# Optimization experiments

Hardware: AMD Instinct MI355X
Metric: run time of the kernel (lower is better)

## Reference

```python
import jax, jax.numpy as jnp
import numpy as np

B, MAXN, F, H, T, L = 32, 1024, 215, 256, 8, 3
N = B * MAXN            # 32768 global nodes
E = 524288              # total edges, global indices


def setup_inputs() -> dict:
    key = jax.random.key(0)
    ks = jax.random.split(key, 12)
    s = 0.05
    return {
        "node_features": jax.random.normal(ks[0], (B, MAXN, F), dtype=jnp.float32),
        "edge_index": jax.random.randint(ks[1], (2, E), 0, N, dtype=jnp.int32),
        "edge_type": jax.random.randint(ks[2], (E,), 0, T, dtype=jnp.int32),
        # input projection
        "Wp": jax.random.normal(ks[3], (H, F), dtype=jnp.float32) * s,
        "bp": jax.random.normal(ks[4], (H,), dtype=jnp.float32) * s,
        # per-layer, per-edge-type message linears
        "Wm": jax.random.normal(ks[5], (L, T, H, H), dtype=jnp.float32) * s,
        "bm": jax.random.normal(ks[6], (L, T, H), dtype=jnp.float32) * s,
        # per-layer GRUCell params (torch layout: [r|z|n] stacked, 3H rows)
        "Wih": jax.random.normal(ks[7], (L, 3 * H, H), dtype=jnp.float32) * s,
        "Whh": jax.random.normal(ks[8], (L, 3 * H, H), dtype=jnp.float32) * s,
        "bih": jax.random.normal(ks[9], (L, 3 * H), dtype=jnp.float32) * s,
        "bhh": jax.random.normal(ks[10], (L, 3 * H), dtype=jnp.float32) * s,
    }


def _gru_cell(x, h, Wih, Whh, bih, bhh):
    # torch.nn.GRUCell math
    gi = x @ Wih.T + bih            # (N, 3H)
    gh = h @ Whh.T + bhh            # (N, 3H)
    i_r, i_z, i_n = jnp.split(gi, 3, axis=-1)
    h_r, h_z, h_n = jnp.split(gh, 3, axis=-1)
    r = jax.nn.sigmoid(i_r + h_r)
    z = jax.nn.sigmoid(i_z + h_z)
    n = jnp.tanh(i_n + r * h_n)
    return (1.0 - z) * n + z * h


def reference(node_features, edge_index, edge_type, Wp, bp, Wm, bm, Wih, Whh, bih, bhh):
    # flatten batch of graphs into global node array, project to hidden
    h = node_features.reshape(-1, F) @ Wp.T + bp          # (N, H)
    src, dst = edge_index[0], edge_index[1]
    for l in range(L):
        # apply all T type-specific linears to every node once (equivalent to
        # the per-edge-type mask+gather+Linear loop), then gather per edge
        Ht = jnp.einsum('nd,ted->nte', h, Wm[l]) + bm[l]  # (N, T, H)
        msg = Ht[src, edge_type]                           # (E, H) gather
        m = jax.ops.segment_sum(msg, dst, num_segments=N)  # scatter-add (N, H)
        h = _gru_cell(m, h, Wih[l], Whh[l], bih[l], bhh[l])
        # dropout is identity in eval mode
    # readout: full graphs -> sum each graph's node block
    return h.reshape(B, MAXN, H).sum(axis=1)               # (B, H)
```

## Files before the change

### kernel.cpp

```cpp
#include <hip/hip_runtime.h>

#define N_NODES 32768
#define E_EDGES 524288
#define F_IN    215
#define H_DIM   256
#define T_TYPES 8
#define L_LAYERS 3
#define B_GRAPHS 32
#define MAXN_   1024
#define NT_BINS (N_NODES * T_TYPES)

typedef float  f32x4  __attribute__((ext_vector_type(4)));
typedef __bf16 bf16x8 __attribute__((ext_vector_type(8)));

__device__ __forceinline__ unsigned short f2bf(float f) {
  union { float f; unsigned u; } v; v.f = f;
  unsigned r = v.u + 0x7fffu + ((v.u >> 16) & 1u);
  return (unsigned short)(r >> 16);
}
__device__ __forceinline__ float bf2f(unsigned short h) {
  union { unsigned u; float f; } v; v.u = ((unsigned)h) << 16;
  return v.f;
}
__device__ __forceinline__ float bflo(unsigned u) { union { unsigned x; float f; } v; v.x = u << 16; return v.f; }
__device__ __forceinline__ float bfhi(unsigned u) { union { unsigned x; float f; } v; v.x = u & 0xffff0000u; return v.f; }

typedef const __attribute__((address_space(1))) unsigned int* gas_ptr;
typedef __attribute__((address_space(3))) unsigned int* las_ptr;
__device__ __forceinline__ void gload_lds16(const unsigned short* g, unsigned short* l) {
  __builtin_amdgcn_global_load_lds((gas_ptr)g, (las_ptr)l, 16, 0, 0);
}

__device__ __forceinline__ void acc16(float* a, const uint4 v, const uint4 w) {
  a[0]  += bflo(v.x); a[1]  += bfhi(v.x);
  a[2]  += bflo(v.y); a[3]  += bfhi(v.y);
  a[4]  += bflo(v.z); a[5]  += bfhi(v.z);
  a[6]  += bflo(v.w); a[7]  += bfhi(v.w);
  a[8]  += bflo(w.x); a[9]  += bfhi(w.x);
  a[10] += bflo(w.y); a[11] += bfhi(w.y);
  a[12] += bflo(w.z); a[13] += bfhi(w.z);
  a[14] += bflo(w.w); a[15] += bfhi(w.w);
}

static constexpr size_t OFF_BIG     = 0;
static constexpr size_t REL_CURSOR  = 1048576;
static constexpr size_t REL_BSUM    = 2097152;
static constexpr size_t REL_WPPAD   = 33554432;
static constexpr size_t REL_HALT    = 50331648;
static constexpr size_t REL_OFFS    = 100663296;
static constexpr size_t REL_SORTED  = 104857600;
static constexpr size_t OFF_H_B     = 134217728;
static constexpr size_t OFF_M_B     = 150994944;
static constexpr size_t OFF_WMB     = 167772160;
static constexpr size_t OFF_WIH     = 170917888;
static constexpr size_t OFF_WHH     = 172097536;
static constexpr size_t WS_REQUIRED = 173277184;

__global__ void hist_kernel(const int* __restrict__ dst, const int* __restrict__ et,
                            int* __restrict__ cnt) {
  int e = blockIdx.x * 256 + threadIdx.x;
  atomicAdd(&cnt[dst[e] * T_TYPES + et[e]], 1);
}

__global__ __launch_bounds__(1024) void scan1(const int* __restrict__ cnt,
                                              int* __restrict__ offs,
                                              int* __restrict__ bsum) {
  __shared__ int wsum[16];
  const int t = threadIdx.x, lane = t & 63, wid = t >> 6;
  const int idx = blockIdx.x * 1024 + t;
  const int v = cnt[idx];
  int x = v;
  #pragma unroll
  for (int off = 1; off < 64; off <<= 1) {
    int u = __shfl_up(x, off, 64);
    if (lane >= off) x += u;
  }
  if (lane == 63) wsum[wid] = x;
  __syncthreads();
  int wbase = 0;
  for (int i = 0; i < wid; ++i) wbase += wsum[i];
  offs[idx] = wbase + x - v;
  if (t == 1023) bsum[blockIdx.x] = wbase + x;
}

__global__ __launch_bounds__(256) void scan2(int* __restrict__ bsum) {
  __shared__ int wsum[4];
  const int t = threadIdx.x, lane = t & 63, wid = t >> 6;
  const int v = bsum[t];
  int x = v;
  #pragma unroll
  for (int off = 1; off < 64; off <<= 1) {
    int u = __shfl_up(x, off, 64);
    if (lane >= off) x += u;
  }
  if (lane == 63) wsum[wid] = x;
  __syncthreads();
  int wbase = 0;
  for (int i = 0; i < wid; ++i) wbase += wsum[i];
  __syncthreads();
  bsum[t] = wbase + x - v;
}

__global__ __launch_bounds__(1024) void scan3(int* __restrict__ offs,
                                              const int* __restrict__ bsum,
                                              int* __restrict__ cursor) {
  const int idx = blockIdx.x * 1024 + threadIdx.x;
  const int o = offs[idx] + bsum[blockIdx.x];
  offs[idx] = o;
  cursor[idx] = o;
  if (idx == 0) offs[NT_BINS] = E_EDGES;
}

__global__ void reorder_kernel(const int* __restrict__ src, const int* __restrict__ dst,
                               const int* __restrict__ et, int* __restrict__ cursor,
                               unsigned short* __restrict__ sorted) {
  int e = blockIdx.x * 256 + threadIdx.x;
  int key = dst[e] * T_TYPES + et[e];
  int p = atomicAdd(&cursor[key], 1);
  sorted[p] = (unsigned short)src[e];
}

__global__ void cvt_f32_bf16(const float* __restrict__ in, unsigned short* __restrict__ out, int n) {
  int i = blockIdx.x * 256 + threadIdx.x;
  if (i < n) out[i] = f2bf(in[i]);
}

__global__ void pad_cvt(const float* __restrict__ in, unsigned short* __restrict__ out,
                        int rows, int cin) {
  int i = blockIdx.x * 256 + threadIdx.x;
  if (i >= rows * 256) return;
  int r = i >> 8, c = i & 255;
  out[i] = (c < cin) ? f2bf(in[(size_t)r * cin + c]) : (unsigned short)0;
}

__global__ __launch_bounds__(256, 2) void gemm_bt(
    const unsigned short* __restrict__ A,
    const unsigned short* __restrict__ W,
    const float* __restrict__ bias,
    unsigned short* __restrict__ C,
    int M, int K) {
  __shared__ unsigned short As[128 * 32];
  __shared__ unsigned short Bs[128 * 32];
  const int tid = threadIdx.x;
  const int lane = tid & 63;
  const int wv = tid >> 6;
  const int lrow = lane & 15;
  const int lquad = lane >> 4;
  const int bm0 = blockIdx.x * 128;
  const int bn0 = blockIdx.y * 128;
  const int srow = wv * 16 + (lane >> 2);
  const int scol = (lane & 3) * 8;

  f32x4 acc[2][8] = {};

  for (int kt = 0; kt < K; kt += 32) {
    #pragma unroll
    for (int i = 0; i < 2; ++i) {
      const int row = srow + i * 64;
      gload_lds16(A + (size_t)(bm0 + row) * K + kt + scol, &As[row * 32 + scol]);
      gload_lds16(W + (size_t)(bn0 + row) * K + kt + scol, &Bs[row * 32 + scol]);
    }
    __syncthreads();
    bf16x8 af[2], bfr[8];
    #pragma unroll
    for (int mt = 0; mt < 2; ++mt)
      af[mt] = *(const bf16x8*)(&As[(wv * 32 + mt * 16 + lrow) * 32 + lquad * 8]);
    #pragma unroll
    for (int nt = 0; nt < 8; ++nt)
      bfr[nt] = *(const bf16x8*)(&Bs[(nt * 16 + lrow) * 32 + lquad * 8]);
    #pragma unroll
    for (int mt = 0; mt < 2; ++mt)
      #pragma unroll
      for (int nt = 0; nt < 8; ++nt)
        acc[mt][nt] = __builtin_amdgcn_mfma_f32_16x16x32_bf16(af[mt], bfr[nt], acc[mt][nt], 0, 0, 0);
    __syncthreads();
  }

  #pragma unroll
  for (int mt = 0; mt < 2; ++mt) {
    #pragma unroll
    for (int r = 0; r < 4; ++r) {
      const int grow = bm0 + wv * 32 + mt * 16 + lquad * 4 + r;
      #pragma unroll
      for (int nt = 0; nt < 8; ++nt) {
        const int gcol = bn0 + nt * 16 + lrow;
        float v = acc[mt][nt][r] + (bias ? bias[gcol] : 0.f);
        C[(size_t)grow * M + gcol] = f2bf(v);
      }
    }
  }
}

__global__ __launch_bounds__(512, 4) void msg_gemm(
    const int* __restrict__ offs, const unsigned short* __restrict__ sorted,
    const unsigned short* __restrict__ hb, const unsigned short* __restrict__ Wt_l,
    const float* __restrict__ bm_l, unsigned short* __restrict__ m) {
  constexpr int CH = 2568;
  __shared__ unsigned short Ss[8 * CH];
  __shared__ unsigned short Bs[2][256 * 32];
  __shared__ unsigned short idxS[2048];
  __shared__ int offsS[516];
  const int tid = threadIdx.x;
  const int lane = tid & 63;
  const int wv = tid >> 6;
  const int lrow = lane & 15;
  const int lquad = lane >> 4;
  const int wrow = wv & 3;
  const int wcol = wv >> 2;
  const int bm0 = blockIdx.x * 64;
  const int gg = wv * 4 + lquad;
  const int brow = tid >> 2;
  const int bcol = (tid & 3) * 8;

  const int gseg0 = offs[bm0 * 8];
  const int gseg1 = offs[bm0 * 8 + 512];
  const int seg = gseg1 - gseg0;
  for (int i = tid; i < 513; i += 512) offsS[i] = offs[bm0 * 8 + i];
  const int segc = seg < 2048 ? seg : 2048;
  for (int i = tid; i < segc; i += 512) idxS[i] = sorted[gseg0 + i];
  const bool useLds = (seg <= 2048);
  const unsigned short* ip = useLds ? (const unsigned short*)idxS : (sorted + gseg0);
  __syncthreads();

  f32x4 acc[8] = {};
  int buf = 0;

  for (int t = 0; t < T_TYPES; ++t) {
    #pragma unroll
    for (int step = 0; step < 2; ++step) {
      const int dloc = gg + step * 32;
      const int beg = offsS[dloc * 8 + t] - gseg0;
      const int end = offsS[dloc * 8 + t + 1] - gseg0;
      float a[16];
      #pragma unroll
      for (int j = 0; j < 16; ++j) a[j] = 0.f;
      int e = beg;
      if (e + 2 <= end) {
        int s0 = ip[e], s1 = ip[e + 1];
        const unsigned short* h0 = hb + (size_t)s0 * H_DIM + lrow * 16;
        const unsigned short* h1 = hb + (size_t)s1 * H_DIM + lrow * 16;
        uint4 pv0 = *(const uint4*)h0, pw0 = *(const uint4*)(h0 + 8);
        uint4 pv1 = *(const uint4*)h1, pw1 = *(const uint4*)(h1 + 8);
        e += 2;
        for (; e + 2 <= end; e += 2) {
          const int n0 = ip[e], n1 = ip[e + 1];
          const unsigned short* g0 = hb + (size_t)n0 * H_DIM + lrow * 16;
          const unsigned short* g1 = hb + (size_t)n1 * H_DIM + lrow * 16;
          const uint4 nv0 = *(const uint4*)g0, nw0 = *(const uint4*)(g0 + 8);
          const uint4 nv1 = *(const uint4*)g1, nw1 = *(const uint4*)(g1 + 8);
          acc16(a, pv0, pw0);
          acc16(a, pv1, pw1);
          pv0 = nv0; pw0 = nw0; pv1 = nv1; pw1 = nw1;
        }
        acc16(a, pv0, pw0);
        acc16(a, pv1, pw1);
      }
      if (e < end) {
        const int s0 = ip[e];
        const unsigned short* h0 = hb + (size_t)s0 * H_DIM + lrow * 16;
        acc16(a, *(const uint4*)h0, *(const uint4*)(h0 + 8));
      }
      union { unsigned short us[16]; uint4 q[2]; } ob;
      #pragma unroll
      for (int j = 0; j < 16; ++j) ob.us[j] = f2bf(a[j]);
      uint4* p = (uint4*)&Ss[(lrow >> 1) * CH + dloc * 40 + (lrow & 1) * 16];
      p[0] = ob.q[0];
      p[1] = ob.q[1];
    }
    const unsigned short* Wt = Wt_l + (size_t)t * 65536;
    gload_lds16(Wt + (size_t)brow * 256 + bcol, &Bs[buf][brow * 32 + bcol]);
    gload_lds16(Wt + (size_t)(brow + 128) * 256 + bcol, &Bs[buf][(brow + 128) * 32 + bcol]);
    __syncthreads();
    for (int kc = 0; kc < 8; ++kc) {
      if (kc < 7) {
        gload_lds16(Wt + (size_t)brow * 256 + (kc + 1) * 32 + bcol,
                    &Bs[buf ^ 1][brow * 32 + bcol]);
        gload_lds16(Wt + (size_t)(brow + 128) * 256 + (kc + 1) * 32 + bcol,
                    &Bs[buf ^ 1][(brow + 128) * 32 + bcol]);
      }
      const bf16x8 af = *(const bf16x8*)(&Ss[kc * CH + (wrow * 16 + lrow) * 40 + lquad * 8]);
      #pragma unroll
      for (int nt = 0; nt < 8; ++nt) {
        const bf16x8 b = *(const bf16x8*)(&Bs[buf][((wcol * 8 + nt) * 16 + lrow) * 32 + lquad * 8]);
        acc[nt] = __builtin_amdgcn_mfma_f32_16x16x32_bf16(af, b, acc[nt], 0, 0, 0);
      }
      buf ^= 1;
      __syncthreads();
    }
  }

  float cnt[4][8];
  #pragma unroll
  for (int r = 0; r < 4; ++r) {
    const int dl = wrow * 16 + lquad * 4 + r;
    #pragma unroll
    for (int t = 0; t < 8; ++t)
      cnt[r][t] = (float)(offsS[dl * 8 + t + 1] - offsS[dl * 8 + t]);
  }
  #pragma unroll
  for (int nt = 0; nt < 8; ++nt) {
    const int gcol = wcol * 128 + nt * 16 + lrow;
    float bmv[8];
    #pragma unroll
    for (int t = 0; t < 8; ++t) bmv[t] = bm_l[t * H_DIM + gcol];
    #pragma unroll
    for (int r = 0; r < 4; ++r) {
      const int grow = bm0 + wrow * 16 + lquad * 4 + r;
      float v = acc[nt][r];
      #pragma unroll
      for (int t = 0; t < 8; ++t) v += cnt[r][t] * bmv[t];
      m[(size_t)grow * H_DIM + gcol] = f2bf(v);
    }
  }
}

__global__ __launch_bounds__(256, 3) void gru_fused(
    const unsigned short* __restrict__ mB,
    const unsigned short* __restrict__ hin,
    const unsigned short* __restrict__ wih_l,
    const unsigned short* __restrict__ whh_l,
    const float* __restrict__ bih_l,
    const float* __restrict__ bhh_l,
    unsigned short* __restrict__ hout) {
  __shared__ unsigned short Am[64 * 32];
  __shared__ unsigned short Ah[64 * 32];
  const int tid = threadIdx.x;
  const int lane = tid & 63;
  const int wv = tid >> 6;
  const int lrow = lane & 15;
  const int lquad = lane >> 4;
  const int n0 = blockIdx.x * 64;
  const int c0 = blockIdx.y * 64;
  const int arow = tid >> 2;
  const int scol = (tid & 3) * 8;

  f32x4 acc[6][4] = {};

  for (int kt = 0; kt < 256; kt += 32) {
    __syncthreads();
    gload_lds16(mB  + (size_t)(n0 + arow) * 256 + kt + scol, &Am[arow * 32 + scol]);
    gload_lds16(hin + (size_t)(n0 + arow) * 256 + kt + scol, &Ah[arow * 32 + scol]);
    __syncthreads();
    const int wr = c0 + wv * 16 + lrow;
    bf16x8 bfr[6];
    #pragma unroll
    for (int g = 0; g < 3; ++g) {
      bfr[g]     = *(const bf16x8*)(wih_l + (size_t)(g * 256 + wr) * 256 + kt + lquad * 8);
      bfr[g + 3] = *(const bf16x8*)(whh_l + (size_t)(g * 256 + wr) * 256 + kt + lquad * 8);
    }
    #pragma unroll
    for (int mt = 0; mt < 4; ++mt) {
      const bf16x8 am = *(const bf16x8*)(&Am[(mt * 16 + lrow) * 32 + lquad * 8]);
      const bf16x8 ah = *(const bf16x8*)(&Ah[(mt * 16 + lrow) * 32 + lquad * 8]);
      #pragma unroll
      for (int g = 0; g < 6; ++g)
        acc[g][mt] = __builtin_amdgcn_mfma_f32_16x16x32_bf16(g < 3 ? am : ah, bfr[g], acc[g][mt], 0, 0, 0);
    }
  }

  const int c = c0 + wv * 16 + lrow;
  const float b_ir = bih_l[c], b_iz = bih_l[256 + c], b_in = bih_l[512 + c];
  const float b_hr = bhh_l[c], b_hz = bhh_l[256 + c], b_hn = bhh_l[512 + c];
  #pragma unroll
  for (int mt = 0; mt < 4; ++mt) {
    #pragma unroll
    for (int r = 0; r < 4; ++r) {
      const int node = n0 + mt * 16 + lquad * 4 + r;
      const float i_r = acc[0][mt][r] + b_ir;
      const float i_z = acc[1][mt][r] + b_iz;
      const float i_n = acc[2][mt][r] + b_in;
      const float h_r = acc[3][mt][r] + b_hr;
      const float h_z = acc[4][mt][r] + b_hz;
      const float h_n = acc[5][mt][r] + b_hn;
      const float rr = 1.f / (1.f + __expf(-(i_r + h_r)));
      const float zz = 1.f / (1.f + __expf(-(i_z + h_z)));
      const float nn = tanhf(i_n + rr * h_n);
      const float hp = bf2f(hin[(size_t)node * 256 + c]);
      hout[(size_t)node * 256 + c] = f2bf((1.f - zz) * nn + zz * hp);
    }
  }
}

__global__ __launch_bounds__(256) void readout_partial(const unsigned short* __restrict__ hb,
                                                       float* __restrict__ part) {
  const int b = blockIdx.x >> 3;
  const int ch = blockIdx.x & 7;
  const int c = threadIdx.x;
  const unsigned short* base = hb + ((size_t)b * MAXN_ + ch * 128) * H_DIM + c;
  float s = 0.f;
  #pragma unroll 4
  for (int i = 0; i < 128; ++i) s += bf2f(base[(size_t)i * H_DIM]);
  part[(size_t)blockIdx.x * H_DIM + c] = s;
}

__global__ __launch_bounds__(256) void readout_final(const float* __restrict__ part,
                                                     float* __restrict__ out) {
  const int b = blockIdx.x;
  const int c = threadIdx.x;
  float s = 0.f;
  #pragma unroll
  for (int i = 0; i < 8; ++i) s += part[((size_t)b * 8 + i) * H_DIM + c];
  out[b * H_DIM + c] = s;
}

extern "C" void kernel_launch(void* const* d_in, const int* in_sizes, int n_in,
                              void* d_out, int out_size, void* d_ws, size_t ws_size,
                              hipStream_t stream) {
  if (ws_size < WS_REQUIRED) return;

  const float* X   = (const float*)d_in[0];
  const int*   ei  = (const int*)d_in[1];
  const int*   et  = (const int*)d_in[2];
  const float* Wp  = (const float*)d_in[3];
  const float* bp  = (const float*)d_in[4];
  const float* Wm  = (const float*)d_in[5];
  const float* bm  = (const float*)d_in[6];
  const float* Wih = (const float*)d_in[7];
  const float* Whh = (const float*)d_in[8];
  const float* bih = (const float*)d_in[9];
  const float* bhh = (const float*)d_in[10];
  float* out = (float*)d_out;
  char* ws = (char*)d_ws;

  int*            counts = (int*)(ws + OFF_BIG);
  int*            cursor = (int*)(ws + OFF_BIG + REL_CURSOR);
  int*            bsum   = (int*)(ws + OFF_BIG + REL_BSUM);
  unsigned short* xpad   = (unsigned short*)(ws + OFF_BIG);
  unsigned short* wppad  = (unsigned short*)(ws + OFF_BIG + REL_WPPAD);
  unsigned short* h_alt  = (unsigned short*)(ws + OFF_BIG + REL_HALT);
  float*          part   = (float*)(ws + OFF_BIG);
  int*            offs   = (int*)(ws + OFF_BIG + REL_OFFS);
  unsigned short* sorted = (unsigned short*)(ws + OFF_BIG + REL_SORTED);
  unsigned short* h_b    = (unsigned short*)(ws + OFF_H_B);
  unsigned short* m_b    = (unsigned short*)(ws + OFF_M_B);
  unsigned short* wmb    = (unsigned short*)(ws + OFF_WMB);
  unsigned short* wih_b  = (unsigned short*)(ws + OFF_WIH);
  unsigned short* whh_b  = (unsigned short*)(ws + OFF_WHH);

  const int* src = ei;
  const int* dst = ei + E_EDGES;

  hipMemsetAsync(counts, 0, NT_BINS * sizeof(int), stream);
  hist_kernel<<<E_EDGES / 256, 256, 0, stream>>>(dst, et, counts);
  scan1<<<NT_BINS / 1024, 1024, 0, stream>>>(counts, offs, bsum);
  scan2<<<1, 256, 0, stream>>>(bsum);
  scan3<<<NT_BINS / 1024, 1024, 0, stream>>>(offs, bsum, cursor);
  reorder_kernel<<<E_EDGES / 256, 256, 0, stream>>>(src, dst, et, cursor, sorted);

  pad_cvt<<<(N_NODES * 256) / 256, 256, 0, stream>>>(X, xpad, N_NODES, F_IN);
  pad_cvt<<<(256 * 256) / 256, 256, 0, stream>>>(Wp, wppad, 256, F_IN);
  cvt_f32_bf16<<<(L_LAYERS * T_TYPES * H_DIM * H_DIM) / 256, 256, 0, stream>>>(
      Wm, wmb, L_LAYERS * T_TYPES * H_DIM * H_DIM);
  cvt_f32_bf16<<<(L_LAYERS * 3 * H_DIM * H_DIM) / 256, 256, 0, stream>>>(Wih, wih_b, L_LAYERS * 3 * H_DIM * H_DIM);
  cvt_f32_bf16<<<(L_LAYERS * 3 * H_DIM * H_DIM) / 256, 256, 0, stream>>>(Whh, whh_b, L_LAYERS * 3 * H_DIM * H_DIM);

  gemm_bt<<<dim3(N_NODES / 128, 2), 256, 0, stream>>>(xpad, wppad, bp, h_b, H_DIM, 256);

  for (int l = 0; l < L_LAYERS; ++l) {
    const unsigned short* wm_l  = wmb + (size_t)l * T_TYPES * H_DIM * H_DIM;
    const unsigned short* wih_l = wih_b + (size_t)l * 3 * H_DIM * H_DIM;
    const unsigned short* whh_l = whh_b + (size_t)l * 3 * H_DIM * H_DIM;
    const float* bm_l  = bm + (size_t)l * T_TYPES * H_DIM;
    const float* bih_l = bih + (size_t)l * 3 * H_DIM;
    const float* bhh_l = bhh + (size_t)l * 3 * H_DIM;

    unsigned short* h_cur = (l & 1) ? h_alt : h_b;
    unsigned short* h_nxt = (l & 1) ? h_b : h_alt;

    msg_gemm<<<N_NODES / 64, 512, 0, stream>>>(offs, sorted, h_cur, wm_l, bm_l, m_b);
    gru_fused<<<dim3(N_NODES / 64, 4), 256, 0, stream>>>(
        m_b, h_cur, wih_l, whh_l, bih_l, bhh_l, h_nxt);
  }

  readout_partial<<<B_GRAPHS * 8, 256, 0, stream>>>(h_alt, part);
  readout_final<<<B_GRAPHS, 256, 0, stream>>>(part, out);

  (void)in_sizes; (void)n_in; (void)out_size;
}
```

Before: 628.2 us.

## Retile GRU kernel to full-width rows and fuse weight conversion launches

The GRU kernel now has each block handle 32 nodes across all 256 output columns, with each wave covering 64 columns. Before, each block handled 64 nodes by 64 columns, so the same m/h rows were reloaded four times across blockIdx.y. The r and z gates now sum the input and hidden contributions in one shared accumulator, which cuts accumulator registers, and launch bounds drop to 2 blocks per CU. The three weight conversion kernels are merged into one launch to save launch overhead. In exchange, each wave streams more weight rows per node tile, which means more B-operand global loads per MFMA.

```diff
diff --git a/kernel.cpp b/kernel.cpp
--- a/kernel.cpp
+++ b/kernel.cpp
@@ -120,9 +120,17 @@
   sorted[p] = (unsigned short)src[e];
 }
 
-__global__ void cvt_f32_bf16(const float* __restrict__ in, unsigned short* __restrict__ out, int n) {
+__global__ void cvt_weights(const float* __restrict__ a, const float* __restrict__ b,
+                            const float* __restrict__ c,
+                            unsigned short* __restrict__ oa, unsigned short* __restrict__ ob,
+                            unsigned short* __restrict__ oc,
+                            int na, int nb, int nc) {
   int i = blockIdx.x * 256 + threadIdx.x;
-  if (i < n) out[i] = f2bf(in[i]);
+  if (i < na) { oa[i] = f2bf(a[i]); return; }
+  int j = i - na;
+  if (j < nb) { ob[j] = f2bf(b[j]); return; }
+  int k = j - nb;
+  if (k < nc) oc[k] = f2bf(c[k]);
 }
 
 __global__ void pad_cvt(const float* __restrict__ in, unsigned short* __restrict__ out,
@@ -314,7 +322,7 @@
   }
 }
 
-__global__ __launch_bounds__(256, 3) void gru_fused(
+__global__ __launch_bounds__(256, 2) void gru_fused(
     const unsigned short* __restrict__ mB,
     const unsigned short* __restrict__ hin,
     const unsigned short* __restrict__ wih_l,
@@ -322,61 +330,69 @@
     const float* __restrict__ bih_l,
     const float* __restrict__ bhh_l,
     unsigned short* __restrict__ hout) {
-  __shared__ unsigned short Am[64 * 32];
-  __shared__ unsigned short Ah[64 * 32];
+  __shared__ unsigned short Am[32 * 32];
+  __shared__ unsigned short Ah[32 * 32];
   const int tid = threadIdx.x;
   const int lane = tid & 63;
   const int wv = tid >> 6;
   const int lrow = lane & 15;
   const int lquad = lane >> 4;
-  const int n0 = blockIdx.x * 64;
-  const int c0 = blockIdx.y * 64;
-  const int arow = tid >> 2;
+  const int n0 = blockIdx.x * 32;
+  const int c0 = wv * 64;
+  const int srow = (tid & 127) >> 2;
   const int scol = (tid & 3) * 8;
 
-  f32x4 acc[6][4] = {};
+  f32x4 racc[2][4] = {}, zacc[2][4] = {}, nacc[2][4] = {}, hnacc[2][4] = {};
 
   for (int kt = 0; kt < 256; kt += 32) {
     __syncthreads();
-    gload_lds16(mB  + (size_t)(n0 + arow) * 256 + kt + scol, &Am[arow * 32 + scol]);
-    gload_lds16(hin + (size_t)(n0 + arow) * 256 + kt + scol, &Ah[arow * 32 + scol]);
+    if (tid < 128) gload_lds16(mB  + (size_t)(n0 + srow) * 256 + kt + scol, &Am[srow * 32 + scol]);
+    else           gload_lds16(hin + (size_t)(n0 + srow) * 256 + kt + scol, &Ah[srow * 32 + scol]);
     __syncthreads();
-    const int wr = c0 + wv * 16 + lrow;
-    bf16x8 bfr[6];
-    #pragma unroll
-    for (int g = 0; g < 3; ++g) {
-      bfr[g]     = *(const bf16x8*)(wih_l + (size_t)(g * 256 + wr) * 256 + kt + lquad * 8);
-      bfr[g + 3] = *(const bf16x8*)(whh_l + (size_t)(g * 256 + wr) * 256 + kt + lquad * 8);
-    }
-    #pragma unroll
-    for (int mt = 0; mt < 4; ++mt) {
-      const bf16x8 am = *(const bf16x8*)(&Am[(mt * 16 + lrow) * 32 + lquad * 8]);
-      const bf16x8 ah = *(const bf16x8*)(&Ah[(mt * 16 + lrow) * 32 + lquad * 8]);
-      #pragma unroll
-      for (int g = 0; g < 6; ++g)
-        acc[g][mt] = __builtin_amdgcn_mfma_f32_16x16x32_bf16(g < 3 ? am : ah, bfr[g], acc[g][mt], 0, 0, 0);
-    }
-  }
-
-  const int c = c0 + wv * 16 + lrow;
-  const float b_ir = bih_l[c], b_iz = bih_l[256 + c], b_in = bih_l[512 + c];
-  const float b_hr = bhh_l[c], b_hz = bhh_l[256 + c], b_hn = bhh_l[512 + c];
-  #pragma unroll
-  for (int mt = 0; mt < 4; ++mt) {
-    #pragma unroll
-    for (int r = 0; r < 4; ++r) {
-      const int node = n0 + mt * 16 + lquad * 4 + r;
-      const float i_r = acc[0][mt][r] + b_ir;
-      const float i_z = acc[1][mt][r] + b_iz;
-      const float i_n = acc[2][mt][r] + b_in;
-      const float h_r = acc[3][mt][r] + b_hr;
-      const float h_z = acc[4][mt][r] + b_hz;
-      const float h_n = acc[5][mt][r] + b_hn;
-      const float rr = 1.f / (1.f + __expf(-(i_r + h_r)));
-      const float zz = 1.f / (1.f + __expf(-(i_z + h_z)));
-      const float nn = tanhf(i_n + rr * h_n);
-      const float hp = bf2f(hin[(size_t)node * 256 + c]);
-      hout[(size_t)node * 256 + c] = f2bf((1.f - zz) * nn + zz * hp);
+    bf16x8 am[2], ah[2];
+    #pragma unroll
+    for (int mt = 0; mt < 2; ++mt) {
+      am[mt] = *(const bf16x8*)(&Am[(mt * 16 + lrow) * 32 + lquad * 8]);
+      ah[mt] = *(const bf16x8*)(&Ah[(mt * 16 + lrow) * 32 + lquad * 8]);
+    }
+    #pragma unroll
+    for (int nt = 0; nt < 4; ++nt) {
+      const int wr = c0 + nt * 16 + lrow;
+      const size_t ko = kt + lquad * 8;
+      const bf16x8 bir = *(const bf16x8*)(wih_l + (size_t)(0 * 256 + wr) * 256 + ko);
+      const bf16x8 biz = *(const bf16x8*)(wih_l + (size_t)(1 * 256 + wr) * 256 + ko);
+      const bf16x8 bin_ = *(const bf16x8*)(wih_l + (size_t)(2 * 256 + wr) * 256 + ko);
+      const bf16x8 bhr = *(const bf16x8*)(whh_l + (size_t)(0 * 256 + wr) * 256 + ko);
+      const bf16x8 bhz = *(const bf16x8*)(whh_l + (size_t)(1 * 256 + wr) * 256 + ko);
+      const bf16x8 bhn = *(const bf16x8*)(whh_l + (size_t)(2 * 256 + wr) * 256 + ko);
+      #pragma unroll
+      for (int mt = 0; mt < 2; ++mt) {
+        racc[mt][nt]  = __builtin_amdgcn_mfma_f32_16x16x32_bf16(am[mt], bir,  racc[mt][nt], 0, 0, 0);
+        zacc[mt][nt]  = __builtin_amdgcn_mfma_f32_16x16x32_bf16(am[mt], biz,  zacc[mt][nt], 0, 0, 0);
+        nacc[mt][nt]  = __builtin_amdgcn_mfma_f32_16x16x32_bf16(am[mt], bin_, nacc[mt][nt], 0, 0, 0);
+        racc[mt][nt]  = __builtin_amdgcn_mfma_f32_16x16x32_bf16(ah[mt], bhr,  racc[mt][nt], 0, 0, 0);
+        zacc[mt][nt]  = __builtin_amdgcn_mfma_f32_16x16x32_bf16(ah[mt], bhz,  zacc[mt][nt], 0, 0, 0);
+        hnacc[mt][nt] = __builtin_amdgcn_mfma_f32_16x16x32_bf16(ah[mt], bhn,  hnacc[mt][nt], 0, 0, 0);
+      }
+    }
+  }
+
+  #pragma unroll
+  for (int nt = 0; nt < 4; ++nt) {
+    const int c = c0 + nt * 16 + lrow;
+    const float b_ir = bih_l[c], b_iz = bih_l[256 + c], b_in = bih_l[512 + c];
+    const float b_hr = bhh_l[c], b_hz = bhh_l[256 + c], b_hn = bhh_l[512 + c];
+    #pragma unroll
+    for (int mt = 0; mt < 2; ++mt) {
+      #pragma unroll
+      for (int r = 0; r < 4; ++r) {
+        const int node = n0 + mt * 16 + lquad * 4 + r;
+        const float rr = 1.f / (1.f + __expf(-(racc[mt][nt][r] + b_ir + b_hr)));
+        const float zz = 1.f / (1.f + __expf(-(zacc[mt][nt][r] + b_iz + b_hz)));
+        const float nn = tanhf(nacc[mt][nt][r] + b_in + rr * (hnacc[mt][nt][r] + b_hn));
+        const float hp = bf2f(hin[(size_t)node * 256 + c]);
+        hout[(size_t)node * 256 + c] = f2bf((1.f - zz) * nn + zz * hp);
+      }
     }
   }
 }
@@ -449,10 +465,13 @@
 
   pad_cvt<<<(N_NODES * 256) / 256, 256, 0, stream>>>(X, xpad, N_NODES, F_IN);
   pad_cvt<<<(256 * 256) / 256, 256, 0, stream>>>(Wp, wppad, 256, F_IN);
-  cvt_f32_bf16<<<(L_LAYERS * T_TYPES * H_DIM * H_DIM) / 256, 256, 0, stream>>>(
-      Wm, wmb, L_LAYERS * T_TYPES * H_DIM * H_DIM);
-  cvt_f32_bf16<<<(L_LAYERS * 3 * H_DIM * H_DIM) / 256, 256, 0, stream>>>(Wih, wih_b, L_LAYERS * 3 * H_DIM * H_DIM);
-  cvt_f32_bf16<<<(L_LAYERS * 3 * H_DIM * H_DIM) / 256, 256, 0, stream>>>(Whh, whh_b, L_LAYERS * 3 * H_DIM * H_DIM);
+  {
+    const int na = L_LAYERS * T_TYPES * H_DIM * H_DIM;
+    const int nb = L_LAYERS * 3 * H_DIM * H_DIM;
+    const int nc = nb;
+    cvt_weights<<<(na + nb + nc + 255) / 256, 256, 0, stream>>>(
+        Wm, Wih, Whh, wmb, wih_b, whh_b, na, nb, nc);
+  }
 
   gemm_bt<<<dim3(N_NODES / 128, 2), 256, 0, stream>>>(xpad, wppad, bp, h_b, H_DIM, 256);
 
@@ -468,7 +487,7 @@
     unsigned short* h_nxt = (l & 1) ? h_b : h_alt;
 
     msg_gemm<<<N_NODES / 64, 512, 0, stream>>>(offs, sorted, h_cur, wm_l, bm_l, m_b);
-    gru_fused<<<dim3(N_NODES / 64, 4), 256, 0, stream>>>(
+    gru_fused<<<N_NODES / 32, 256, 0, stream>>>(
         m_b, h_cur, wih_l, whh_l, bih_l, bhh_l, h_nxt);
   }
 
```

After: 784.4 us. 24.9% more time.
